# Kernel optimization log

Measured on AMD Instinct MI355X. Metric: run time of the kernel, lower is better.

Reference implementation:

```python
import jax, jax.numpy as jnp
import numpy as np

N, E, IN, H, OUT = 100000, 1600000, 128, 128, 64


def setup_inputs() -> dict:
    key = jax.random.key(0)
    ks = jax.random.split(key, 6)
    glorot = lambda k, i, o: jax.random.normal(k, (i, o), jnp.float32) * np.float32(np.sqrt(2.0 / (i + o)))
    return dict(
        x=jax.random.normal(ks[0], (N, IN), jnp.float32),
        edge_index=jax.random.randint(ks[1], (2, E), 0, N, dtype=jnp.int64 if jax.config.jax_enable_x64 else jnp.int32),
        W1=glorot(ks[2], IN, H), b1=jnp.zeros((H,), jnp.float32),
        W2=glorot(ks[3], H, H), b2=jnp.zeros((H,), jnp.float32),
        W3=glorot(ks[4], H, OUT), b3=jnp.zeros((OUT,), jnp.float32),
    )


def _gcn_norm(edge_index, num_nodes):
    # add self loops with weight 1.0 (GCNConv add_self_loops=True, edge_weight=None -> ones)
    loop = jnp.arange(num_nodes, dtype=edge_index.dtype)
    src = jnp.concatenate([edge_index[0], loop])
    dst = jnp.concatenate([edge_index[1], loop])
    ew = jnp.ones(src.shape, jnp.float32)
    deg = jax.ops.segment_sum(ew, dst, num_segments=num_nodes)  # in-degree on dst
    dinv = jnp.where(deg > 0, jax.lax.rsqrt(deg), 0.0)
    norm = dinv[src] * ew * dinv[dst]  # [E+N]
    return src, dst, norm


def _conv(x, src, dst, norm, W, b):
    h = x @ W                                        # linear transform first (GCNConv order)
    msg = h[src] * norm[:, None]                     # gather + scale, [E+N, F]
    agg = jax.ops.segment_sum(msg, dst, num_segments=x.shape[0])  # scatter-add
    return agg + b


def reference(x, edge_index, W1, b1, W2, b2, W3, b3):
    # eval-mode forward: dropout is identity
    src, dst, norm = _gcn_norm(edge_index, x.shape[0])  # same graph -> norm shared across layers
    h = jax.nn.relu(_conv(x, src, dst, norm, W1, b1))
    h = jax.nn.relu(_conv(h, src, dst, norm, W2, b2))
    h = _conv(h, src, dst, norm, W3, b3)
    return jax.nn.log_softmax(h, axis=-1)
```

## Files before the change

kernel.cpp:

```cpp
#include <hip/hip_runtime.h>

typedef unsigned int u32;
typedef unsigned short u16;
typedef unsigned char u8;
typedef long i64;
typedef __attribute__((ext_vector_type(8))) short short8;
typedef __attribute__((ext_vector_type(4))) float f32x4;

#define MAXBIN 1024
#define SORT_TPB 1024
#define BINCAP 4096
#define CSRCAP 5120

__device__ inline u16 f2bf(float f) {
    u32 u = __builtin_bit_cast(u32, f);
    u32 r = (u + 0x7fffu + ((u >> 16) & 1u)) >> 16;
    return (u16)r;
}

__device__ inline f32x4 mfma_fp8(uint2 a, uint2 b, f32x4 c) {
    return __builtin_amdgcn_mfma_f32_16x16x32_fp8_fp8(
        __builtin_bit_cast(i64, a), __builtin_bit_cast(i64, b), c, 0, 0, 0);
}

__device__ inline int permP(int p) {
    return ((p >> 5) << 5) + ((p & 3) << 3) + ((p >> 2) & 7);
}

__global__ __launch_bounds__(SORT_TPB) void k_bscatter(const int* __restrict__ ei, int E, int W,
                                                       int* __restrict__ binCnt,
                                                       u32* __restrict__ binned, int NBIN) {
    __shared__ int lh[MAXBIN];
    __shared__ int lb[MAXBIN];
    int tid = threadIdx.x;
    for (int i = tid; i < NBIN; i += SORT_TPB) lh[i] = 0;
    __syncthreads();
    int s = blockIdx.x * W, e = min(E, s + W);
    for (int j = s + tid; j < e; j += SORT_TPB) atomicAdd(&lh[ei[E + j] >> 7], 1);
    __syncthreads();
    for (int i = tid; i < NBIN; i += SORT_TPB) {
        int h = lh[i];
        int base = 0;
        if (h) {
            base = atomicAdd(&binCnt[i], h);
            if (base + h > BINCAP) base = BINCAP - h;
        }
        lb[i] = i * BINCAP + base;
    }
    __syncthreads();
    for (int i = tid; i < NBIN; i += SORT_TPB) lh[i] = 0;
    __syncthreads();
    for (int j = s + tid; j < e; j += SORT_TPB) {
        int d = ei[E + j];
        int b = d >> 7;
        int r = atomicAdd(&lh[b], 1);
        binned[lb[b] + r] = ((u32)ei[j] << 7) | (u32)(d & 127);
    }
}

__global__ __launch_bounds__(256) void k_bcsr(const u32* __restrict__ binned,
                                              const int* __restrict__ binCnt,
                                              int N, int* __restrict__ offs,
                                              int* __restrict__ ends,
                                              float* __restrict__ dinv,
                                              int* __restrict__ csr) {
    __shared__ int cnt[128];
    __shared__ int off[128];
    __shared__ int tot;
    __shared__ int fillEnd;
    int b = blockIdx.x;
    int tid = threadIdx.x;
    int dLo = b << 7;
    int nd = min(128, N - dLo);
    int bbase = b * BINCAP;
    int gCnt = min(binCnt[b], BINCAP);
    int pbase = b * CSRCAP;
    if (tid < 128) cnt[tid] = 0;
    __syncthreads();
    for (int j = tid; j < gCnt; j += 256) atomicAdd(&cnt[binned[bbase + j] & 127u], 1);
    __syncthreads();
    int c = (tid < 128) ? cnt[tid] : 0;
    int pc = (tid < 128) ? ((c + 8) & ~7) : 0;
    int lane = tid & 63;
    int isc = pc;
    for (int d = 1; d < 64; d <<= 1) { int o = __shfl_up(isc, d, 64); if (lane >= d) isc += o; }
    if (tid == 63) tot = isc;
    __syncthreads();
    int add = (tid >= 64 && tid < 128) ? tot : 0;
    if (tid < 128) off[tid] = add + isc - pc;
    if (tid == 127) fillEnd = add + isc;
    __syncthreads();
    for (int j = tid; j < fillEnd; j += 256) csr[pbase + j] = N;
    __syncthreads();
    if (tid < nd) {
        offs[dLo + tid] = pbase + off[tid];
        ends[dLo + tid] = pbase + off[tid] + pc;
        dinv[dLo + tid] = rsqrtf((float)(c + 1));
        csr[pbase + off[tid] + c] = dLo + tid;
    }
    if (tid < 128) cnt[tid] = 0;
    __syncthreads();
    for (int j = tid; j < gCnt; j += 256) {
        u32 v = binned[bbase + j];
        int d7 = (int)(v & 127u);
        int r = atomicAdd(&cnt[d7], 1);
        csr[pbase + off[d7] + r] = (int)(v >> 7);
    }
}

__global__ void k_wtall(const float* __restrict__ W1, const float* __restrict__ W2,
                        const float* __restrict__ W3, u16* __restrict__ wt1,
                        u16* __restrict__ wt2, u16* __restrict__ wt3) {
    int idx = blockIdx.x * 256 + threadIdx.x;
    if (idx < 16384) {
        int k = idx >> 7, m = idx & 127;
        wt1[m * 128 + k] = f2bf(W1[idx]);
    } else if (idx < 32768) {
        int i = idx - 16384, p = i >> 7, m = i & 127;
        wt2[m * 128 + p] = f2bf(W2[permP(p) * 128 + m]);
    } else if (idx < 40960) {
        int i = idx - 32768, p = i >> 6, m = i & 63;
        wt3[m * 128 + p] = f2bf(W3[permP(p) * 64 + m]);
    }
}

template <int M, bool F32IN>
__global__ __launch_bounds__(256) void k_gemm(const void* __restrict__ xin,
                                              const u16* __restrict__ wt,
                                              const float* __restrict__ dinv,
                                              u8* __restrict__ g8, int N) {
    constexpr int K = 128;
    constexpr int LDK = 136;
    __shared__ u16 lwt[M * LDK];
    int tid = threadIdx.x;
    if (blockIdx.x == 0 && tid < M / 16)
        *(uint4*)(g8 + (size_t)N * M + (size_t)tid * 16) = make_uint4(0u, 0u, 0u, 0u);
    const uint4* wsrc = (const uint4*)wt;
#pragma unroll
    for (int c = tid; c < M * K / 8; c += 256) {
        int row = c >> 4, kc = c & 15;
        *(uint4*)&lwt[row * LDK + kc * 8] = wsrc[c];
    }
    __syncthreads();
    int lane = tid & 63, wv = tid >> 6;
    int node = blockIdx.x * 64 + wv * 16 + (lane & 15);
    int nodec = min(node, N - 1);
    int kr = (lane >> 4) * 8;
    f32x4 acc[M / 16];
#pragma unroll
    for (int t = 0; t < M / 16; t++) acc[t] = (f32x4){0.f, 0.f, 0.f, 0.f};
#pragma unroll
    for (int ks = 0; ks < 4; ks++) {
        short8 bfr;
        if (F32IN) {
            const float* xr = (const float*)xin + (size_t)nodec * K + ks * 32 + kr;
            float4 fa = *(const float4*)xr;
            float4 fb = *(const float4*)(xr + 4);
            bfr = (short8){(short)f2bf(fa.x), (short)f2bf(fa.y), (short)f2bf(fa.z),
                           (short)f2bf(fa.w), (short)f2bf(fb.x), (short)f2bf(fb.y),
                           (short)f2bf(fb.z), (short)f2bf(fb.w)};
        } else {
            bfr = *(const short8*)((const u16*)xin + (size_t)nodec * K + ks * 32 + kr);
        }
#pragma unroll
        for (int t = 0; t < M / 16; t++) {
            short8 afr = *(const short8*)&lwt[(t * 16 + (lane & 15)) * LDK + ks * 32 + kr];
            acc[t] = __builtin_amdgcn_mfma_f32_16x16x32_bf16(afr, bfr, acc[t], 0, 0, 0);
        }
    }
    if (node < N) {
        float dv16 = dinv[node] * 16.0f;
        int r0 = (lane >> 4) * 4;
#pragma unroll
        for (int t = 0; t < M / 16; t++) {
            u32 w = __builtin_amdgcn_cvt_pk_fp8_f32(acc[t][0] * dv16, acc[t][1] * dv16, 0, false);
            w = __builtin_amdgcn_cvt_pk_fp8_f32(acc[t][2] * dv16, acc[t][3] * dv16, w, true);
            *(u32*)(g8 + (size_t)node * M + t * 16 + r0) = w;
        }
    }
}

__global__ __launch_bounds__(256) void k_agg128(const u8* __restrict__ g8,
                                                const int* __restrict__ offs,
                                                const int* __restrict__ ends,
                                                const int* __restrict__ csr,
                                                const float* __restrict__ dinv,
                                                const float* __restrict__ bias,
                                                u16* __restrict__ hout, int N) {
    int wp = (blockIdx.x * 256 + threadIdx.x) >> 6;
    int widA = wp * 2;
    if (widA >= N) return;
    int widB = widA + 1;
    bool hasB = widB < N;
    int lane = threadIdx.x & 63;
    int q = lane >> 4;
    int f = lane & 15;
    int sA = offs[widA], eA = ends[widA];
    int sB = hasB ? offs[widB] : 0;
    int eB = hasB ? ends[widB] : 0;
    int nn = f & 7;
    bool on = (f < 8) ? (q < 2) : (q >= 2);
    uint2 bsel;
    bsel.x = (on && nn < 4) ? (0x38u << (8 * nn)) : 0u;
    bsel.y = (on && nn >= 4) ? (0x38u << (8 * (nn - 4))) : 0u;
    const u8* gf = g8 + f * 8;
    bool isA = (q < 2);
    int qm = q & 1;
    f32x4 ac0 = {0.f, 0.f, 0.f, 0.f}, ac1 = ac0, ac2 = ac0, ac3 = ac0;
    int jA = sA, jB = sB;
    while (jA < eA || jB < eB) {
        bool okA = jA < eA, okB = jB < eB;
        int base = isA ? jA : jB;
        bool ok = isA ? okA : okB;
        int i0 = csr[base + qm];
        int i1 = csr[base + 2 + qm];
        int i2 = csr[base + 4 + qm];
        int i3 = csr[base + 6 + qm];
        if (!ok) { i0 = N; i1 = N; i2 = N; i3 = N; }
        uint2 w0 = *(const uint2*)(gf + ((u32)i0 << 7));
        uint2 w1 = *(const uint2*)(gf + ((u32)i1 << 7));
        uint2 w2 = *(const uint2*)(gf + ((u32)i2 << 7));
        uint2 w3 = *(const uint2*)(gf + ((u32)i3 << 7));
        ac0 = mfma_fp8(w0, bsel, ac0);
        ac1 = mfma_fp8(w1, bsel, ac1);
        ac2 = mfma_fp8(w2, bsel, ac2);
        ac3 = mfma_fp8(w3, bsel, ac3);
        if (okA) jA += 8;
        if (okB) jB += 8;
    }
    f32x4 a = (ac0 + ac1) + (ac2 + ac3);
    int jn = lane & 15, fq = lane >> 4;
    int node = (jn < 8) ? widA : widB;
    if (node < N) {
        float sc = dinv[node] * 0.0625f;
        int bb = (jn & 7);
        u32 o0, o1;
        {
            float v0 = fmaxf(fmaf(a[0], sc, bias[(4 * fq + 0) * 8 + bb]), 0.f);
            float v1 = fmaxf(fmaf(a[1], sc, bias[(4 * fq + 1) * 8 + bb]), 0.f);
            o0 = (u32)f2bf(v0) | ((u32)f2bf(v1) << 16);
        }
        {
            float v2 = fmaxf(fmaf(a[2], sc, bias[(4 * fq + 2) * 8 + bb]), 0.f);
            float v3 = fmaxf(fmaf(a[3], sc, bias[(4 * fq + 3) * 8 + bb]), 0.f);
            o1 = (u32)f2bf(v2) | ((u32)f2bf(v3) << 16);
        }
        *(uint2*)&hout[(size_t)node * 128 + fq * 32 + bb * 4] = make_uint2(o0, o1);
    }
}

__global__ __launch_bounds__(256) void k_agg64(const u8* __restrict__ g8,
                                               const int* __restrict__ offs,
                                               const int* __restrict__ ends,
                                               const int* __restrict__ csr,
                                               const float* __restrict__ dinv,
                                               const float* __restrict__ bias,
                                               float* __restrict__ out, int N) {
    __shared__ float sm[4][2][64];
    int wp = (blockIdx.x * 256 + threadIdx.x) >> 6;
    int widA = wp * 2;
    if (widA >= N) return;
    int widB = widA + 1;
    bool hasB = widB < N;
    int lane = threadIdx.x & 63;
    int wv = (int)(threadIdx.x >> 6);
    int q = lane >> 4;
    int f = lane & 15;
    bool isA = (f < 8);
    int sA = offs[widA], eA = ends[widA];
    int sB = hasB ? offs[widB] : 0;
    int eB = hasB ? ends[widB] : 0;
    uint2 bsel;
    bsel.x = (f < 4) ? (0x38u << (8 * f)) : 0u;
    bsel.y = (f >= 4 && f < 8) ? (0x38u << (8 * (f - 4))) : 0u;
    const u8* gf = g8 + (f & 7) * 8;
    f32x4 ac0 = {0.f, 0.f, 0.f, 0.f}, ac1 = ac0;
    int jA = sA, jB = sB;
    while (jA < eA || jB < eB) {
        bool okA = jA < eA, okB = jB < eB;
        int base = isA ? jA : jB;
        bool ok = isA ? okA : okB;
        int i0 = csr[base + q];
        int i1 = csr[base + 4 + q];
        if (!ok) { i0 = N; i1 = N; }
        uint2 w0 = *(const uint2*)(gf + ((u32)i0 << 6));
        uint2 w1 = *(const uint2*)(gf + ((u32)i1 << 6));
        ac0 = mfma_fp8(w0, bsel, ac0);
        ac1 = mfma_fp8(w1, bsel, ac1);
        if (okA) jA += 8;
        if (okB) jB += 8;
    }
    f32x4 a = ac0 + ac1;
    int jn = lane & 15, fq = lane >> 4;
    int half = fq >> 1;
    int node = widA + half;
    bool act = (jn < 8) && (node < N);
    if (act) {
        float sc = dinv[node] * 0.0625f;
        int ch = (fq & 1);
        float v0 = fmaf(a[0], sc, bias[(4 * ch + 0) * 8 + jn]);
        float v1 = fmaf(a[1], sc, bias[(4 * ch + 1) * 8 + jn]);
        float v2 = fmaf(a[2], sc, bias[(4 * ch + 2) * 8 + jn]);
        float v3 = fmaf(a[3], sc, bias[(4 * ch + 3) * 8 + jn]);
        float m = fmaxf(fmaxf(v0, v1), fmaxf(v2, v3));
        m = fmaxf(m, __shfl_xor(m, 1, 64));
        m = fmaxf(m, __shfl_xor(m, 2, 64));
        m = fmaxf(m, __shfl_xor(m, 4, 64));
        m = fmaxf(m, __shfl_xor(m, 16, 64));
        float ss = __expf(v0 - m) + __expf(v1 - m) + __expf(v2 - m) + __expf(v3 - m);
        ss += __shfl_xor(ss, 1, 64);
        ss += __shfl_xor(ss, 2, 64);
        ss += __shfl_xor(ss, 4, 64);
        ss += __shfl_xor(ss, 16, 64);
        float lg = m + __logf(ss);
        sm[wv][half][(4 * ch + 0) * 8 + jn] = v0 - lg;
        sm[wv][half][(4 * ch + 1) * 8 + jn] = v1 - lg;
        sm[wv][half][(4 * ch + 2) * 8 + jn] = v2 - lg;
        sm[wv][half][(4 * ch + 3) * 8 + jn] = v3 - lg;
    }
    if (lane < 32) {
        int h = lane >> 4;
        int node2 = widA + h;
        if (node2 < N) {
            float4 ov = *(float4*)&sm[wv][h][(lane & 15) * 4];
            *(float4*)&out[(size_t)node2 * 64 + (lane & 15) * 4] = ov;
        }
    }
}

extern "C" void kernel_launch(void* const* d_in, const int* in_sizes, int n_in,
                              void* d_out, int out_size, void* d_ws, size_t ws_size,
                              hipStream_t stream) {
    const float* x  = (const float*)d_in[0];
    const int*   ei = (const int*)d_in[1];
    const float* W1 = (const float*)d_in[2];
    const float* b1 = (const float*)d_in[3];
    const float* W2 = (const float*)d_in[4];
    const float* b2 = (const float*)d_in[5];
    const float* W3 = (const float*)d_in[6];
    const float* b3 = (const float*)d_in[7];
    const int N = in_sizes[0] / 128;
    const int E = in_sizes[1] / 2;
    const int NBIN = (N + 127) >> 7;

    char* ws = (char*)d_ws;
    size_t o = 0;
    auto alloc = [&](size_t bytes) -> char* {
        char* p = ws + o;
        o += (bytes + 255) & ~(size_t)255;
        return p;
    };
    int*   binCnt = (int*)alloc((size_t)MAXBIN * 4);
    float* dinv   = (float*)alloc((size_t)N * 4);
    int*   offs   = (int*)alloc((size_t)N * 4);
    int*   endsA  = (int*)alloc((size_t)N * 4);
    int*   csr    = (int*)alloc(((size_t)NBIN * CSRCAP + 64) * 4);
    u16*   wt1    = (u16*)alloc(128 * 128 * 2);
    u16*   wt2    = (u16*)alloc(128 * 128 * 2);
    u16*   wt3    = (u16*)alloc(64 * 128 * 2);
    u8*    g8     = (u8*)alloc(((size_t)N + 1) * 128);
    u16*   hbuf   = (u16*)alloc((size_t)N * 128 * 2);
    u32*   binned = (u32*)hbuf;
    float* outp   = (float*)d_out;

    hipMemsetAsync(binCnt, 0, (size_t)MAXBIN * 4, stream);
    int W256 = (E + 255) / 256;
    k_bscatter<<<256, SORT_TPB, 0, stream>>>(ei, E, W256, binCnt, binned, NBIN);
    k_bcsr<<<NBIN, 256, 0, stream>>>(binned, binCnt, N, offs, endsA, dinv, csr);
    k_wtall<<<(40960 + 255) / 256, 256, 0, stream>>>(W1, W2, W3, wt1, wt2, wt3);

    int gG = (N + 63) / 64;
    int P  = (N + 1) / 2;
    int gA = (P + 3) / 4;

    k_gemm<128, true ><<<gG, 256, 0, stream>>>(x,    wt1, dinv, g8, N);
    k_agg128<<<gA, 256, 0, stream>>>(g8, offs, endsA, csr, dinv, b1, hbuf, N);
    k_gemm<128, false><<<gG, 256, 0, stream>>>(hbuf, wt2, dinv, g8, N);
    k_agg128<<<gA, 256, 0, stream>>>(g8, offs, endsA, csr, dinv, b2, hbuf, N);
    k_gemm<64,  false><<<gG, 256, 0, stream>>>(hbuf, wt3, dinv, g8, N);
    k_agg64<<<gA, 256, 0, stream>>>(g8, offs, endsA, csr, dinv, b3, outp, N);
}
```

Before: 277.8 us.

## Make aggregation waves persistent over node pairs and prefetch next pair's CSR data

The aggregation kernels now have each wave loop over several node pairs (PPW=4) in a grid-stride pattern instead of one pair per wave. While the current pair is processed, the next pair's offsets/ends and its first batch of neighbor indices are loaded early, hiding the dependent index-load latency at the start of each pair. This cuts the grid to a quarter of the waves, which can lower occupancy-based latency hiding and worsen load balance for high-degree nodes.

```diff
diff --git a/kernel.cpp b/kernel.cpp
--- a/kernel.cpp
+++ b/kernel.cpp
@@ -11,6 +11,7 @@
 #define SORT_TPB 1024
 #define BINCAP 4096
 #define CSRCAP 5120
+#define PPW 4
 
 __device__ inline u16 f2bf(float f) {
     u32 u = __builtin_bit_cast(u32, f);
@@ -186,18 +187,12 @@
                                                 const int* __restrict__ csr,
                                                 const float* __restrict__ dinv,
                                                 const float* __restrict__ bias,
-                                                u16* __restrict__ hout, int N) {
-    int wp = (blockIdx.x * 256 + threadIdx.x) >> 6;
-    int widA = wp * 2;
-    if (widA >= N) return;
-    int widB = widA + 1;
-    bool hasB = widB < N;
+                                                u16* __restrict__ hout, int N, int P, int NW) {
+    int wv0 = (blockIdx.x * 256 + threadIdx.x) >> 6;
+    if (wv0 >= NW || wv0 >= P) return;
     int lane = threadIdx.x & 63;
     int q = lane >> 4;
     int f = lane & 15;
-    int sA = offs[widA], eA = ends[widA];
-    int sB = hasB ? offs[widB] : 0;
-    int eB = hasB ? ends[widB] : 0;
     int nn = f & 7;
     bool on = (f < 8) ? (q < 2) : (q >= 2);
     uint2 bsel;
@@ -206,46 +201,91 @@
     const u8* gf = g8 + f * 8;
     bool isA = (q < 2);
     int qm = q & 1;
-    f32x4 ac0 = {0.f, 0.f, 0.f, 0.f}, ac1 = ac0, ac2 = ac0, ac3 = ac0;
-    int jA = sA, jB = sB;
-    while (jA < eA || jB < eB) {
-        bool okA = jA < eA, okB = jB < eB;
-        int base = isA ? jA : jB;
-        bool ok = isA ? okA : okB;
-        int i0 = csr[base + qm];
-        int i1 = csr[base + 2 + qm];
-        int i2 = csr[base + 4 + qm];
-        int i3 = csr[base + 6 + qm];
-        if (!ok) { i0 = N; i1 = N; i2 = N; i3 = N; }
-        uint2 w0 = *(const uint2*)(gf + ((u32)i0 << 7));
-        uint2 w1 = *(const uint2*)(gf + ((u32)i1 << 7));
-        uint2 w2 = *(const uint2*)(gf + ((u32)i2 << 7));
-        uint2 w3 = *(const uint2*)(gf + ((u32)i3 << 7));
-        ac0 = mfma_fp8(w0, bsel, ac0);
-        ac1 = mfma_fp8(w1, bsel, ac1);
-        ac2 = mfma_fp8(w2, bsel, ac2);
-        ac3 = mfma_fp8(w3, bsel, ac3);
-        if (okA) jA += 8;
-        if (okB) jB += 8;
-    }
-    f32x4 a = (ac0 + ac1) + (ac2 + ac3);
-    int jn = lane & 15, fq = lane >> 4;
-    int node = (jn < 8) ? widA : widB;
-    if (node < N) {
-        float sc = dinv[node] * 0.0625f;
-        int bb = (jn & 7);
-        u32 o0, o1;
+    int wp = wv0;
+    int widA = wp * 2, widB = widA + 1;
+    int sA = offs[widA], eA = ends[widA];
+    int sB = (widB < N) ? offs[widB] : 0;
+    int eB = (widB < N) ? ends[widB] : 0;
+    int base0 = isA ? sA : sB;
+    int p0 = csr[base0 + qm];
+    int p1 = csr[base0 + 2 + qm];
+    int p2 = csr[base0 + 4 + qm];
+    int p3 = csr[base0 + 6 + qm];
+    while (true) {
+        f32x4 ac0 = {0.f, 0.f, 0.f, 0.f}, ac1 = ac0, ac2 = ac0, ac3 = ac0;
+        int jA = sA, jB = sB;
         {
-            float v0 = fmaxf(fmaf(a[0], sc, bias[(4 * fq + 0) * 8 + bb]), 0.f);
-            float v1 = fmaxf(fmaf(a[1], sc, bias[(4 * fq + 1) * 8 + bb]), 0.f);
-            o0 = (u32)f2bf(v0) | ((u32)f2bf(v1) << 16);
-        }
-        {
-            float v2 = fmaxf(fmaf(a[2], sc, bias[(4 * fq + 2) * 8 + bb]), 0.f);
-            float v3 = fmaxf(fmaf(a[3], sc, bias[(4 * fq + 3) * 8 + bb]), 0.f);
-            o1 = (u32)f2bf(v2) | ((u32)f2bf(v3) << 16);
-        }
-        *(uint2*)&hout[(size_t)node * 128 + fq * 32 + bb * 4] = make_uint2(o0, o1);
+            bool okA = jA < eA, okB = jB < eB;
+            bool ok = isA ? okA : okB;
+            int i0 = p0, i1 = p1, i2 = p2, i3 = p3;
+            if (!ok) { i0 = N; i1 = N; i2 = N; i3 = N; }
+            uint2 w0 = *(const uint2*)(gf + ((u32)i0 << 7));
+            uint2 w1 = *(const uint2*)(gf + ((u32)i1 << 7));
+            uint2 w2 = *(const uint2*)(gf + ((u32)i2 << 7));
+            uint2 w3 = *(const uint2*)(gf + ((u32)i3 << 7));
+            ac0 = mfma_fp8(w0, bsel, ac0);
+            ac1 = mfma_fp8(w1, bsel, ac1);
+            ac2 = mfma_fp8(w2, bsel, ac2);
+            ac3 = mfma_fp8(w3, bsel, ac3);
+            if (okA) jA += 8;
+            if (okB) jB += 8;
+        }
+        int wpn = wp + NW;
+        int sAn = 0, eAn = 0, sBn = 0, eBn = 0;
+        int widAn = wpn * 2, widBn = widAn + 1;
+        if (wpn < P) {
+            sAn = offs[widAn]; eAn = ends[widAn];
+            if (widBn < N) { sBn = offs[widBn]; eBn = ends[widBn]; }
+        }
+        while (jA < eA || jB < eB) {
+            bool okA = jA < eA, okB = jB < eB;
+            int base = isA ? jA : jB;
+            bool ok = isA ? okA : okB;
+            int i0 = csr[base + qm];
+            int i1 = csr[base + 2 + qm];
+            int i2 = csr[base + 4 + qm];
+            int i3 = csr[base + 6 + qm];
+            if (!ok) { i0 = N; i1 = N; i2 = N; i3 = N; }
+            uint2 w0 = *(const uint2*)(gf + ((u32)i0 << 7));
+            uint2 w1 = *(const uint2*)(gf + ((u32)i1 << 7));
+            uint2 w2 = *(const uint2*)(gf + ((u32)i2 << 7));
+            uint2 w3 = *(const uint2*)(gf + ((u32)i3 << 7));
+            ac0 = mfma_fp8(w0, bsel, ac0);
+            ac1 = mfma_fp8(w1, bsel, ac1);
+            ac2 = mfma_fp8(w2, bsel, ac2);
+            ac3 = mfma_fp8(w3, bsel, ac3);
+            if (okA) jA += 8;
+            if (okB) jB += 8;
+        }
+        if (wpn < P) {
+            int base0n = isA ? sAn : sBn;
+            p0 = csr[base0n + qm];
+            p1 = csr[base0n + 2 + qm];
+            p2 = csr[base0n + 4 + qm];
+            p3 = csr[base0n + 6 + qm];
+        }
+        f32x4 a = (ac0 + ac1) + (ac2 + ac3);
+        int jn = lane & 15, fq = lane >> 4;
+        int node = (jn < 8) ? widA : widB;
+        if (node < N) {
+            float sc = dinv[node] * 0.0625f;
+            int bb = (jn & 7);
+            u32 o0, o1;
+            {
+                float v0 = fmaxf(fmaf(a[0], sc, bias[(4 * fq + 0) * 8 + bb]), 0.f);
+                float v1 = fmaxf(fmaf(a[1], sc, bias[(4 * fq + 1) * 8 + bb]), 0.f);
+                o0 = (u32)f2bf(v0) | ((u32)f2bf(v1) << 16);
+            }
+            {
+                float v2 = fmaxf(fmaf(a[2], sc, bias[(4 * fq + 2) * 8 + bb]), 0.f);
+                float v3 = fmaxf(fmaf(a[3], sc, bias[(4 * fq + 3) * 8 + bb]), 0.f);
+                o1 = (u32)f2bf(v2) | ((u32)f2bf(v3) << 16);
+            }
+            *(uint2*)&hout[(size_t)node * 128 + fq * 32 + bb * 4] = make_uint2(o0, o1);
+        }
+        if (wpn >= P) break;
+        wp = wpn; widA = widAn; widB = widBn;
+        sA = sAn; eA = eAn; sB = sBn; eB = eBn;
     }
 }
 
@@ -255,76 +295,107 @@
                                                const int* __restrict__ csr,
                                                const float* __restrict__ dinv,
                                                const float* __restrict__ bias,
-                                               float* __restrict__ out, int N) {
+                                               float* __restrict__ out, int N, int P, int NW) {
     __shared__ float sm[4][2][64];
-    int wp = (blockIdx.x * 256 + threadIdx.x) >> 6;
-    int widA = wp * 2;
-    if (widA >= N) return;
-    int widB = widA + 1;
-    bool hasB = widB < N;
+    int wv0 = (blockIdx.x * 256 + threadIdx.x) >> 6;
+    if (wv0 >= NW || wv0 >= P) return;
     int lane = threadIdx.x & 63;
     int wv = (int)(threadIdx.x >> 6);
     int q = lane >> 4;
     int f = lane & 15;
     bool isA = (f < 8);
-    int sA = offs[widA], eA = ends[widA];
-    int sB = hasB ? offs[widB] : 0;
-    int eB = hasB ? ends[widB] : 0;
     uint2 bsel;
     bsel.x = (f < 4) ? (0x38u << (8 * f)) : 0u;
     bsel.y = (f >= 4 && f < 8) ? (0x38u << (8 * (f - 4))) : 0u;
     const u8* gf = g8 + (f & 7) * 8;
-    f32x4 ac0 = {0.f, 0.f, 0.f, 0.f}, ac1 = ac0;
-    int jA = sA, jB = sB;
-    while (jA < eA || jB < eB) {
-        bool okA = jA < eA, okB = jB < eB;
-        int base = isA ? jA : jB;
-        bool ok = isA ? okA : okB;
-        int i0 = csr[base + q];
-        int i1 = csr[base + 4 + q];
-        if (!ok) { i0 = N; i1 = N; }
-        uint2 w0 = *(const uint2*)(gf + ((u32)i0 << 6));
-        uint2 w1 = *(const uint2*)(gf + ((u32)i1 << 6));
-        ac0 = mfma_fp8(w0, bsel, ac0);
-        ac1 = mfma_fp8(w1, bsel, ac1);
-        if (okA) jA += 8;
-        if (okB) jB += 8;
-    }
-    f32x4 a = ac0 + ac1;
-    int jn = lane & 15, fq = lane >> 4;
-    int half = fq >> 1;
-    int node = widA + half;
-    bool act = (jn < 8) && (node < N);
-    if (act) {
-        float sc = dinv[node] * 0.0625f;
-        int ch = (fq & 1);
-        float v0 = fmaf(a[0], sc, bias[(4 * ch + 0) * 8 + jn]);
-        float v1 = fmaf(a[1], sc, bias[(4 * ch + 1) * 8 + jn]);
-        float v2 = fmaf(a[2], sc, bias[(4 * ch + 2) * 8 + jn]);
-        float v3 = fmaf(a[3], sc, bias[(4 * ch + 3) * 8 + jn]);
-        float m = fmaxf(fmaxf(v0, v1), fmaxf(v2, v3));
-        m = fmaxf(m, __shfl_xor(m, 1, 64));
-        m = fmaxf(m, __shfl_xor(m, 2, 64));
-        m = fmaxf(m, __shfl_xor(m, 4, 64));
-        m = fmaxf(m, __shfl_xor(m, 16, 64));
-        float ss = __expf(v0 - m) + __expf(v1 - m) + __expf(v2 - m) + __expf(v3 - m);
-        ss += __shfl_xor(ss, 1, 64);
-        ss += __shfl_xor(ss, 2, 64);
-        ss += __shfl_xor(ss, 4, 64);
-        ss += __shfl_xor(ss, 16, 64);
-        float lg = m + __logf(ss);
-        sm[wv][half][(4 * ch + 0) * 8 + jn] = v0 - lg;
-        sm[wv][half][(4 * ch + 1) * 8 + jn] = v1 - lg;
-        sm[wv][half][(4 * ch + 2) * 8 + jn] = v2 - lg;
-        sm[wv][half][(4 * ch + 3) * 8 + jn] = v3 - lg;
-    }
-    if (lane < 32) {
-        int h = lane >> 4;
-        int node2 = widA + h;
-        if (node2 < N) {
-            float4 ov = *(float4*)&sm[wv][h][(lane & 15) * 4];
-            *(float4*)&out[(size_t)node2 * 64 + (lane & 15) * 4] = ov;
-        }
+    int wp = wv0;
+    int widA = wp * 2, widB = widA + 1;
+    int sA = offs[widA], eA = ends[widA];
+    int sB = (widB < N) ? offs[widB] : 0;
+    int eB = (widB < N) ? ends[widB] : 0;
+    int base0 = isA ? sA : sB;
+    int p0 = csr[base0 + q];
+    int p1 = csr[base0 + 4 + q];
+    while (true) {
+        f32x4 ac0 = {0.f, 0.f, 0.f, 0.f}, ac1 = ac0;
+        int jA = sA, jB = sB;
+        {
+            bool okA = jA < eA, okB = jB < eB;
+            bool ok = isA ? okA : okB;
+            int i0 = p0, i1 = p1;
+            if (!ok) { i0 = N; i1 = N; }
+            uint2 w0 = *(const uint2*)(gf + ((u32)i0 << 6));
+            uint2 w1 = *(const uint2*)(gf + ((u32)i1 << 6));
+            ac0 = mfma_fp8(w0, bsel, ac0);
+            ac1 = mfma_fp8(w1, bsel, ac1);
+            if (okA) jA += 8;
+            if (okB) jB += 8;
+        }
+        int wpn = wp + NW;
+        int sAn = 0, eAn = 0, sBn = 0, eBn = 0;
+        int widAn = wpn * 2, widBn = widAn + 1;
+        if (wpn < P) {
+            sAn = offs[widAn]; eAn = ends[widAn];
+            if (widBn < N) { sBn = offs[widBn]; eBn = ends[widBn]; }
+        }
+        while (jA < eA || jB < eB) {
+            bool okA = jA < eA, okB = jB < eB;
+            int base = isA ? jA : jB;
+            bool ok = isA ? okA : okB;
+            int i0 = csr[base + q];
+            int i1 = csr[base + 4 + q];
+            if (!ok) { i0 = N; i1 = N; }
+            uint2 w0 = *(const uint2*)(gf + ((u32)i0 << 6));
+            uint2 w1 = *(const uint2*)(gf + ((u32)i1 << 6));
+            ac0 = mfma_fp8(w0, bsel, ac0);
+            ac1 = mfma_fp8(w1, bsel, ac1);
+            if (okA) jA += 8;
+            if (okB) jB += 8;
+        }
+        if (wpn < P) {
+            int base0n = isA ? sAn : sBn;
+            p0 = csr[base0n + q];
+            p1 = csr[base0n + 4 + q];
+        }
+        f32x4 a = ac0 + ac1;
+        int jn = lane & 15, fq = lane >> 4;
+        int half = fq >> 1;
+        int node = widA + half;
+        bool act = (jn < 8) && (node < N);
+        if (act) {
+            float sc = dinv[node] * 0.0625f;
+            int ch = (fq & 1);
+            float v0 = fmaf(a[0], sc, bias[(4 * ch + 0) * 8 + jn]);
+            float v1 = fmaf(a[1], sc, bias[(4 * ch + 1) * 8 + jn]);
+            float v2 = fmaf(a[2], sc, bias[(4 * ch + 2) * 8 + jn]);
+            float v3 = fmaf(a[3], sc, bias[(4 * ch + 3) * 8 + jn]);
+            float m = fmaxf(fmaxf(v0, v1), fmaxf(v2, v3));
+            m = fmaxf(m, __shfl_xor(m, 1, 64));
+            m = fmaxf(m, __shfl_xor(m, 2, 64));
+            m = fmaxf(m, __shfl_xor(m, 4, 64));
+            m = fmaxf(m, __shfl_xor(m, 16, 64));
+            float ss = __expf(v0 - m) + __expf(v1 - m) + __expf(v2 - m) + __expf(v3 - m);
+            ss += __shfl_xor(ss, 1, 64);
+            ss += __shfl_xor(ss, 2, 64);
+            ss += __shfl_xor(ss, 4, 64);
+            ss += __shfl_xor(ss, 16, 64);
+            float lg = m + __logf(ss);
+            sm[wv][half][(4 * ch + 0) * 8 + jn] = v0 - lg;
+            sm[wv][half][(4 * ch + 1) * 8 + jn] = v1 - lg;
+            sm[wv][half][(4 * ch + 2) * 8 + jn] = v2 - lg;
+            sm[wv][half][(4 * ch + 3) * 8 + jn] = v3 - lg;
+        }
+        if (lane < 32) {
+            int h = lane >> 4;
+            int node2 = widA + h;
+            if (node2 < N) {
+                float4 ov = *(float4*)&sm[wv][h][(lane & 15) * 4];
+                *(float4*)&out[(size_t)node2 * 64 + (lane & 15) * 4] = ov;
+            }
+        }
+        if (wpn >= P) break;
+        wp = wpn; widA = widAn; widB = widBn;
+        sA = sAn; eA = eAn; sB = sBn; eB = eBn;
     }
 }
 
@@ -371,12 +442,13 @@
 
     int gG = (N + 63) / 64;
     int P  = (N + 1) / 2;
-    int gA = (P + 3) / 4;
+    int NW = (P + PPW - 1) / PPW;
+    int gA = (NW + 3) / 4;
 
     k_gemm<128, true ><<<gG, 256, 0, stream>>>(x,    wt1, dinv, g8, N);
-    k_agg128<<<gA, 256, 0, stream>>>(g8, offs, endsA, csr, dinv, b1, hbuf, N);
+    k_agg128<<<gA, 256, 0, stream>>>(g8, offs, endsA, csr, dinv, b1, hbuf, N, P, NW);
     k_gemm<128, false><<<gG, 256, 0, stream>>>(hbuf, wt2, dinv, g8, N);
-    k_agg128<<<gA, 256, 0, stream>>>(g8, offs, endsA, csr, dinv, b2, hbuf, N);
+    k_agg128<<<gA, 256, 0, stream>>>(g8, offs, endsA, csr, dinv, b2, hbuf, N, P, NW);
     k_gemm<64,  false><<<gG, 256, 0, stream>>>(hbuf, wt3, dinv, g8, N);
-    k_agg64<<<gA, 256, 0, stream>>>(g8, offs, endsA, csr, dinv, b3, outp, N);
-}
+    k_agg64<<<gA, 256, 0, stream>>>(g8, offs, endsA, csr, dinv, b3, outp, N, P, NW);
+}
```

New measurement: 278.7 us. Within noise of the previous version (+0.3%).

## Fuse next-layer GEMM into aggregation epilogue and fold weight prep into scatter

Applied to the files above, without the earlier changes.

The aggregation kernel for layers 1 and 2 now stages the two bf16 output rows in shared memory and immediately multiplies them by the next layer's weights with MFMA, writing fp8 scaled features directly. This removes the separate GEMM kernels for layers 2 and 3 and the bf16 hidden buffer round trip through global memory. Weight conversion is folded into extra blocks of the bucket-scatter kernel, which drops one launch. The cost is that each wave runs a 16-wide MFMA GEMM where only 2 of 16 columns are useful, and it reads weights from global or cache instead of LDS. A separate buffer is also needed for the ping-pong fp8 features.

```diff
diff --git a/kernel.cpp b/kernel.cpp
--- a/kernel.cpp
+++ b/kernel.cpp
@@ -29,7 +29,27 @@
 
 __global__ __launch_bounds__(SORT_TPB) void k_bscatter(const int* __restrict__ ei, int E, int W,
                                                        int* __restrict__ binCnt,
-                                                       u32* __restrict__ binned, int NBIN) {
+                                                       u32* __restrict__ binned, int NBIN,
+                                                       const float* __restrict__ W1,
+                                                       const float* __restrict__ W2,
+                                                       const float* __restrict__ W3,
+                                                       u16* __restrict__ wt1,
+                                                       u16* __restrict__ wt2,
+                                                       u16* __restrict__ wt3) {
+    if (blockIdx.x >= 256) {
+        int idx = (blockIdx.x - 256) * SORT_TPB + threadIdx.x;
+        if (idx < 16384) {
+            int k = idx >> 7, m = idx & 127;
+            wt1[m * 128 + k] = f2bf(W1[idx]);
+        } else if (idx < 32768) {
+            int i = idx - 16384, p = i >> 7, m = i & 127;
+            wt2[m * 128 + p] = f2bf(W2[permP(p) * 128 + m]);
+        } else if (idx < 40960) {
+            int i = idx - 32768, p = i >> 6, m = i & 63;
+            wt3[m * 128 + p] = f2bf(W3[permP(p) * 64 + m]);
+        }
+        return;
+    }
     __shared__ int lh[MAXBIN];
     __shared__ int lb[MAXBIN];
     int tid = threadIdx.x;
@@ -108,29 +128,11 @@
     }
 }
 
-__global__ void k_wtall(const float* __restrict__ W1, const float* __restrict__ W2,
-                        const float* __restrict__ W3, u16* __restrict__ wt1,
-                        u16* __restrict__ wt2, u16* __restrict__ wt3) {
-    int idx = blockIdx.x * 256 + threadIdx.x;
-    if (idx < 16384) {
-        int k = idx >> 7, m = idx & 127;
-        wt1[m * 128 + k] = f2bf(W1[idx]);
-    } else if (idx < 32768) {
-        int i = idx - 16384, p = i >> 7, m = i & 127;
-        wt2[m * 128 + p] = f2bf(W2[permP(p) * 128 + m]);
-    } else if (idx < 40960) {
-        int i = idx - 32768, p = i >> 6, m = i & 63;
-        wt3[m * 128 + p] = f2bf(W3[permP(p) * 64 + m]);
-    }
-}
-
-template <int M, bool F32IN>
-__global__ __launch_bounds__(256) void k_gemm(const void* __restrict__ xin,
-                                              const u16* __restrict__ wt,
-                                              const float* __restrict__ dinv,
-                                              u8* __restrict__ g8, int N) {
-    constexpr int K = 128;
-    constexpr int LDK = 136;
+__global__ __launch_bounds__(256) void k_gemm1(const float* __restrict__ xin,
+                                               const u16* __restrict__ wt,
+                                               const float* __restrict__ dinv,
+                                               u8* __restrict__ g8, int N) {
+    constexpr int M = 128, K = 128, LDK = 136;
     __shared__ u16 lwt[M * LDK];
     int tid = threadIdx.x;
     if (blockIdx.x == 0 && tid < M / 16)
@@ -151,17 +153,12 @@
     for (int t = 0; t < M / 16; t++) acc[t] = (f32x4){0.f, 0.f, 0.f, 0.f};
 #pragma unroll
     for (int ks = 0; ks < 4; ks++) {
-        short8 bfr;
-        if (F32IN) {
-            const float* xr = (const float*)xin + (size_t)nodec * K + ks * 32 + kr;
-            float4 fa = *(const float4*)xr;
-            float4 fb = *(const float4*)(xr + 4);
-            bfr = (short8){(short)f2bf(fa.x), (short)f2bf(fa.y), (short)f2bf(fa.z),
-                           (short)f2bf(fa.w), (short)f2bf(fb.x), (short)f2bf(fb.y),
-                           (short)f2bf(fb.z), (short)f2bf(fb.w)};
-        } else {
-            bfr = *(const short8*)((const u16*)xin + (size_t)nodec * K + ks * 32 + kr);
-        }
+        const float* xr = xin + (size_t)nodec * K + ks * 32 + kr;
+        float4 fa = *(const float4*)xr;
+        float4 fb = *(const float4*)(xr + 4);
+        short8 bfr = (short8){(short)f2bf(fa.x), (short)f2bf(fa.y), (short)f2bf(fa.z),
+                              (short)f2bf(fa.w), (short)f2bf(fb.x), (short)f2bf(fb.y),
+                              (short)f2bf(fb.z), (short)f2bf(fb.w)};
 #pragma unroll
         for (int t = 0; t < M / 16; t++) {
             short8 afr = *(const short8*)&lwt[(t * 16 + (lane & 15)) * LDK + ks * 32 + kr];
@@ -180,19 +177,26 @@
     }
 }
 
-__global__ __launch_bounds__(256) void k_agg128(const u8* __restrict__ g8,
-                                                const int* __restrict__ offs,
-                                                const int* __restrict__ ends,
-                                                const int* __restrict__ csr,
-                                                const float* __restrict__ dinv,
-                                                const float* __restrict__ bias,
-                                                u16* __restrict__ hout, int N) {
+template <int OUTM>
+__global__ __launch_bounds__(256) void k_fagg(const u8* __restrict__ g8in,
+                                              const int* __restrict__ offs,
+                                              const int* __restrict__ ends,
+                                              const int* __restrict__ csr,
+                                              const float* __restrict__ dinv,
+                                              const float* __restrict__ bias,
+                                              const u16* __restrict__ wt,
+                                              u8* __restrict__ g8out, int N) {
+    __shared__ u16 hs[4][2][128];
+    if (blockIdx.x == 0 && threadIdx.x < OUTM / 16)
+        *(uint4*)(g8out + (size_t)N * OUTM + (size_t)threadIdx.x * 16) =
+            make_uint4(0u, 0u, 0u, 0u);
     int wp = (blockIdx.x * 256 + threadIdx.x) >> 6;
     int widA = wp * 2;
     if (widA >= N) return;
     int widB = widA + 1;
     bool hasB = widB < N;
     int lane = threadIdx.x & 63;
+    int wv = (int)(threadIdx.x >> 6);
     int q = lane >> 4;
     int f = lane & 15;
     int sA = offs[widA], eA = ends[widA];
@@ -203,7 +207,7 @@
     uint2 bsel;
     bsel.x = (on && nn < 4) ? (0x38u << (8 * nn)) : 0u;
     bsel.y = (on && nn >= 4) ? (0x38u << (8 * (nn - 4))) : 0u;
-    const u8* gf = g8 + f * 8;
+    const u8* gf = g8in + f * 8;
     bool isA = (q < 2);
     int qm = q & 1;
     f32x4 ac0 = {0.f, 0.f, 0.f, 0.f}, ac1 = ac0, ac2 = ac0, ac3 = ac0;
@@ -231,9 +235,10 @@
     f32x4 a = (ac0 + ac1) + (ac2 + ac3);
     int jn = lane & 15, fq = lane >> 4;
     int node = (jn < 8) ? widA : widB;
+    int half = (jn < 8) ? 0 : 1;
     if (node < N) {
         float sc = dinv[node] * 0.0625f;
-        int bb = (jn & 7);
+        int bb = jn & 7;
         u32 o0, o1;
         {
             float v0 = fmaxf(fmaf(a[0], sc, bias[(4 * fq + 0) * 8 + bb]), 0.f);
@@ -245,7 +250,29 @@
             float v3 = fmaxf(fmaf(a[3], sc, bias[(4 * fq + 3) * 8 + bb]), 0.f);
             o1 = (u32)f2bf(v2) | ((u32)f2bf(v3) << 16);
         }
-        *(uint2*)&hout[(size_t)node * 128 + fq * 32 + bb * 4] = make_uint2(o0, o1);
+        *(uint2*)&hs[wv][half][fq * 32 + bb * 4] = make_uint2(o0, o1);
+    }
+    int c01 = jn & 1;
+    short8 bf0 = *(const short8*)&hs[wv][c01][0 * 32 + fq * 8];
+    short8 bf1 = *(const short8*)&hs[wv][c01][1 * 32 + fq * 8];
+    short8 bf2 = *(const short8*)&hs[wv][c01][2 * 32 + fq * 8];
+    short8 bf3 = *(const short8*)&hs[wv][c01][3 * 32 + fq * 8];
+    int nodeo = widA + jn;
+    float dv16 = (jn < 2 && nodeo < N) ? dinv[nodeo] * 16.0f : 0.f;
+    const u16* wrow = wt + (size_t)jn * 128 + fq * 8;
+#pragma unroll
+    for (int mt = 0; mt < OUTM / 16; mt++) {
+        f32x4 acc = {0.f, 0.f, 0.f, 0.f};
+        const u16* wmt = wrow + mt * 16 * 128;
+        acc = __builtin_amdgcn_mfma_f32_16x16x32_bf16(*(const short8*)(wmt + 0),   bf0, acc, 0, 0, 0);
+        acc = __builtin_amdgcn_mfma_f32_16x16x32_bf16(*(const short8*)(wmt + 32),  bf1, acc, 0, 0, 0);
+        acc = __builtin_amdgcn_mfma_f32_16x16x32_bf16(*(const short8*)(wmt + 64),  bf2, acc, 0, 0, 0);
+        acc = __builtin_amdgcn_mfma_f32_16x16x32_bf16(*(const short8*)(wmt + 96),  bf3, acc, 0, 0, 0);
+        if (jn < 2 && nodeo < N) {
+            u32 w = __builtin_amdgcn_cvt_pk_fp8_f32(acc[0] * dv16, acc[1] * dv16, 0, false);
+            w = __builtin_amdgcn_cvt_pk_fp8_f32(acc[2] * dv16, acc[3] * dv16, w, true);
+            *(u32*)(g8out + (size_t)nodeo * OUTM + mt * 16 + fq * 4) = w;
+        }
     }
 }
 
@@ -358,25 +385,24 @@
     u16*   wt1    = (u16*)alloc(128 * 128 * 2);
     u16*   wt2    = (u16*)alloc(128 * 128 * 2);
     u16*   wt3    = (u16*)alloc(64 * 128 * 2);
-    u8*    g8     = (u8*)alloc(((size_t)N + 1) * 128);
-    u16*   hbuf   = (u16*)alloc((size_t)N * 128 * 2);
-    u32*   binned = (u32*)hbuf;
+    u8*    g8a    = (u8*)alloc(((size_t)N + 1) * 128);
+    u8*    g8b    = (u8*)alloc((size_t)MAXBIN * BINCAP * 4);
+    u32*   binned = (u32*)g8b;
+    u8*    g8c    = g8a;
     float* outp   = (float*)d_out;
 
     hipMemsetAsync(binCnt, 0, (size_t)MAXBIN * 4, stream);
     int W256 = (E + 255) / 256;
-    k_bscatter<<<256, SORT_TPB, 0, stream>>>(ei, E, W256, binCnt, binned, NBIN);
+    k_bscatter<<<256 + 40, SORT_TPB, 0, stream>>>(ei, E, W256, binCnt, binned, NBIN,
+                                                  W1, W2, W3, wt1, wt2, wt3);
     k_bcsr<<<NBIN, 256, 0, stream>>>(binned, binCnt, N, offs, endsA, dinv, csr);
-    k_wtall<<<(40960 + 255) / 256, 256, 0, stream>>>(W1, W2, W3, wt1, wt2, wt3);
 
     int gG = (N + 63) / 64;
     int P  = (N + 1) / 2;
     int gA = (P + 3) / 4;
 
-    k_gemm<128, true ><<<gG, 256, 0, stream>>>(x,    wt1, dinv, g8, N);
-    k_agg128<<<gA, 256, 0, stream>>>(g8, offs, endsA, csr, dinv, b1, hbuf, N);
-    k_gemm<128, false><<<gG, 256, 0, stream>>>(hbuf, wt2, dinv, g8, N);
-    k_agg128<<<gA, 256, 0, stream>>>(g8, offs, endsA, csr, dinv, b2, hbuf, N);
-    k_gemm<64,  false><<<gG, 256, 0, stream>>>(hbuf, wt3, dinv, g8, N);
-    k_agg64<<<gA, 256, 0, stream>>>(g8, offs, endsA, csr, dinv, b3, outp, N);
-}
+    k_gemm1<<<gG, 256, 0, stream>>>(x, wt1, dinv, g8a, N);
+    k_fagg<128><<<gA, 256, 0, stream>>>(g8a, offs, endsA, csr, dinv, b1, wt2, g8b, N);
+    k_fagg<64 ><<<gA, 256, 0, stream>>>(g8b, offs, endsA, csr, dinv, b2, wt3, g8c, N);
+    k_agg64<<<gA, 256, 0, stream>>>(g8c, offs, endsA, csr, dinv, b3, outp, N);
+}
```

New measurement: 497.1 us. +78.9%, slower.
